# Optimization experiments

Hardware: AMD Instinct MI355X
Metric: run time of the kernel (lower is better)

Reference implementation:

```python
import math
import jax, jax.numpy as jnp
import numpy as np

B, N, D, Pd, L, H = 2, 384, 256, 64, 8, 8
Dh = D // H
VOCAB = 21


def _layernorm(x, w, b, eps=1e-5):
    m = jnp.mean(x, axis=-1, keepdims=True)
    v = jnp.var(x, axis=-1, keepdims=True)
    return (x - m) * jax.lax.rsqrt(v + eps) * w + b


def _safe_norm(v):
    return jnp.sqrt(jnp.sum(v * v, axis=-1, keepdims=True) + 1e-8)


def _rot6d(r6):
    # Zhou et al. 6D rotation -> 3x3 via Gram-Schmidt (rows b1,b2,b3)
    a1, a2 = r6[..., :3], r6[..., 3:6]
    b1 = a1 / _safe_norm(a1)
    a2p = a2 - jnp.sum(b1 * a2, axis=-1, keepdims=True) * b1
    b2 = a2p / _safe_norm(a2p)
    b3 = jnp.cross(b1, b2)
    return jnp.stack([b1, b2, b3], axis=-2)  # [..., 3, 3]


def _pos_enc(n, d):
    pos = jnp.arange(n, dtype=jnp.float32)[:, None]
    div = jnp.exp(jnp.arange(0, d, 2, dtype=jnp.float32) * (-math.log(10000.0) / d))
    ang = pos * div  # [n, d/2]
    return jnp.zeros((n, d), jnp.float32).at[:, 0::2].set(jnp.sin(ang)).at[:, 1::2].set(jnp.cos(ang))


def _se3_frame_attention(Q, K, V, frames):
    # Frame-conditioned attention: dot-product scores biased by squared
    # distance between frame translations (IPA-style point bias).
    t = frames[..., :3, 3]                                   # [B,N,3]
    d2 = jnp.sum((t[:, :, None] - t[:, None, :]) ** 2, -1)   # [B,N,N]
    s = jnp.einsum('bihd,bjhd->bhij', Q, K) / math.sqrt(Dh) - d2[:, None]
    a = jax.nn.softmax(s, axis=-1)
    return jnp.einsum('bhij,bjhd->bihd', a, V)               # [B,N,H,Dh]


def _encode(tokens, tok_emb, emb_ln_w, emb_ln_b, Wq, Wk, Wv, Wo, bo,
            attn_ln_w, attn_ln_b, ff_ln_w, ff_ln_b, W1, b1, W2, b2,
            Wop, bop, relpos_emb, pair_ln_w, pair_ln_b, Wf1, bf1, Wf2, bf2):
    Bb, Nn = tokens.shape
    x = tok_emb[tokens] + _pos_enc(Nn, D)[None]
    x = _layernorm(x, emb_ln_w, emb_ln_b)
    frames = jnp.broadcast_to(jnp.eye(4, dtype=x.dtype), (Bb, Nn, 4, 4))
    pos = jnp.arange(Nn)
    rel = jnp.clip(pos[None, :] - pos[:, None], -64, 64) + 64  # rel[i,j]=pos[j]-pos[i]
    rel_e = relpos_emb[rel]                                    # [N,N,Pd]
    bot = jnp.broadcast_to(jnp.array([0.0, 0.0, 0.0, 1.0], x.dtype), (Bb, Nn, 1, 4))
    for l in range(L):
        # SE3 attention block (dropout = identity in eval)
        Q = (x @ Wq[l]).reshape(Bb, Nn, H, Dh)
        Kh = (x @ Wk[l]).reshape(Bb, Nn, H, Dh)
        Vh = (x @ Wv[l]).reshape(Bb, Nn, H, Dh)
        ao = _se3_frame_attention(Q, Kh, Vh, frames).reshape(Bb, Nn, D)
        x = _layernorm(x + ao @ Wo[l] + bo[l], attn_ln_w[l], attn_ln_b[l])
        # FFN (pre-LN inside the Sequential), residual add
        h = _layernorm(x, ff_ln_w[l], ff_ln_b[l])
        x = x + (jax.nn.gelu(h @ W1[l] + b1[l], approximate=False) @ W2[l] + b2[l])
        # Pair features
        proj = jax.nn.relu(x @ Wop + bop)                      # [B,N,Pd]
        pair = _layernorm(proj[:, :, None] + proj[:, None, :] + rel_e[None],
                          pair_ln_w, pair_ln_b)                # [B,N,N,Pd]
        # Frame head
        feat = jnp.concatenate([x, pair.mean(axis=2)], axis=-1)
        raw = jax.nn.silu(feat @ Wf1 + bf1) @ Wf2 + bf2        # [B,N,9]
        R = _rot6d(raw[..., :6])
        trans = raw[..., 6:]
        top = jnp.concatenate([R, trans[..., None]], axis=-1)  # [B,N,3,4]
        frames = jnp.concatenate([top, bot], axis=-2)          # [B,N,4,4]
    return frames, x


def setup_inputs() -> dict:
    key = jax.random.key(0)
    ks = iter(jax.random.split(key, 16))
    def w(shape, scale):
        return (jax.random.normal(next(ks), shape) * scale).astype(jnp.float32)
    return {
        'tokens': jax.random.randint(next(ks), (B, N), 0, VOCAB, dtype=jnp.int32),
        'tok_emb': w((VOCAB, D), 0.02),
        'emb_ln_w': jnp.ones((D,), jnp.float32), 'emb_ln_b': jnp.zeros((D,), jnp.float32),
        'Wq': w((L, D, D), D ** -0.5), 'Wk': w((L, D, D), D ** -0.5),
        'Wv': w((L, D, D), D ** -0.5), 'Wo': w((L, D, D), D ** -0.5),
        'bo': jnp.zeros((L, D), jnp.float32),
        'attn_ln_w': jnp.ones((L, D), jnp.float32), 'attn_ln_b': jnp.zeros((L, D), jnp.float32),
        'ff_ln_w': jnp.ones((L, D), jnp.float32), 'ff_ln_b': jnp.zeros((L, D), jnp.float32),
        'W1': w((L, D, 4 * D), D ** -0.5), 'b1': jnp.zeros((L, 4 * D), jnp.float32),
        'W2': w((L, 4 * D, D), (4 * D) ** -0.5), 'b2': jnp.zeros((L, D), jnp.float32),
        'Wop': w((D, Pd), D ** -0.5), 'bop': jnp.zeros((Pd,), jnp.float32),
        'relpos_emb': w((129, Pd), 0.02),
        'pair_ln_w': jnp.ones((Pd,), jnp.float32), 'pair_ln_b': jnp.zeros((Pd,), jnp.float32),
        'Wf1': w((D + Pd, 128), (D + Pd) ** -0.5), 'bf1': jnp.zeros((128,), jnp.float32),
        'Wf2': w((128, 9), 128 ** -0.5), 'bf2': jnp.zeros((9,), jnp.float32),
    }


def reference(tokens, tok_emb, emb_ln_w, emb_ln_b, Wq, Wk, Wv, Wo, bo,
              attn_ln_w, attn_ln_b, ff_ln_w, ff_ln_b, W1, b1, W2, b2,
              Wop, bop, relpos_emb, pair_ln_w, pair_ln_b, Wf1, bf1, Wf2, bf2):
    return _encode(tokens, tok_emb, emb_ln_w, emb_ln_b, Wq, Wk, Wv, Wo, bo,
                   attn_ln_w, attn_ln_b, ff_ln_w, ff_ln_b, W1, b1, W2, b2,
                   Wop, bop, relpos_emb, pair_ln_w, pair_ln_b, Wf1, bf1, Wf2, bf2)
```

## Files before the change

kernel.cpp:

```cpp
#include <hip/hip_runtime.h>
#include <hip/hip_bf16.h>
#include <math.h>

#define B_  2
#define N_  384
#define D_  256
#define PD_ 64
#define L_  8
#define H_  8
#define DH_ 32
#define GR  4
#define IT  8
#define RT_ 132

__global__ void prologue_kernel(const int* __restrict__ tokens, const float* __restrict__ tok_emb,
                                const float* __restrict__ lnw, const float* __restrict__ lnb,
                                const float* __restrict__ relpos,
                                float* __restrict__ x, float* __restrict__ frames,
                                float* __restrict__ tx, float* __restrict__ ty,
                                float* __restrict__ tz,
                                float* __restrict__ relc, float* __restrict__ relcT) {
  int row = blockIdx.x;
  int n = row % N_;
  int d = threadIdx.x;
  __shared__ float rbuf[256];
  __shared__ float smr;
  if (d < 16) frames[row * 16 + d] = (d == 0 || d == 5 || d == 10 || d == 15) ? 1.0f : 0.0f;
  if (d == 16) tx[row] = 0.0f;
  if (d == 17) ty[row] = 0.0f;
  if (d == 18) tz[row] = 0.0f;
  if (row < 129 && d >= 192) {
    int lane = d & 63;
    float s = relpos[row * PD_ + lane];
    #pragma unroll
    for (int off = 32; off >= 1; off >>= 1) s += __shfl_xor(s, off, 64);
    if (lane == 0) smr = s * (1.0f / PD_);
  }
  int tok = tokens[row];
  float val = tok_emb[tok * D_ + d];
  int i = d >> 1;
  float dv = expf((float)(2 * i) * (-logf(10000.0f) / (float)D_));
  float ang = (float)n * dv;
  val += (d & 1) ? cosf(ang) : sinf(ang);
  rbuf[d] = val; __syncthreads();
  for (int s = 128; s > 0; s >>= 1) { if (d < s) rbuf[d] += rbuf[d + s]; __syncthreads(); }
  float mean = rbuf[0] / D_;
  __syncthreads();
  rbuf[d] = val * val; __syncthreads();
  for (int s = 128; s > 0; s >>= 1) { if (d < s) rbuf[d] += rbuf[d + s]; __syncthreads(); }
  float var = rbuf[0] / D_ - mean * mean;
  float r = rsqrtf(var + 1e-5f);
  x[row * D_ + d] = (val - mean) * r * lnw[d] + lnb[d];
  if (row < 129 && d < PD_) {
    float cv = relpos[row * PD_ + d] - smr;
    relc[row * PD_ + d] = cv;
    relcT[d * RT_ + row] = cv;
  }
}

__device__ __forceinline__ void qkv_unit(int bid, int tid, const float* __restrict__ x,
                                         const float* __restrict__ Wq, const float* __restrict__ Wk,
                                         const float* __restrict__ Wv,
                                         float* __restrict__ q, float* __restrict__ kt,
                                         float* __restrict__ v, float* sA) {
  int tile = bid & 3;
  int m = (bid >> 2) % 3;
  int r0 = (bid / 12) * GR;
  float* red = sA + GR * D_;
  {
    int r = tid >> 6, lane = tid & 63;
    ((float4*)(sA + r * D_))[lane] = ((const float4*)(x + (size_t)(r0 + r) * D_))[lane];
  }
  __syncthreads();
  const float* W = (m == 0) ? Wq : (m == 1) ? Wk : Wv;
  int kc = tid >> 6, c = tid & 63;
  const float* wp = W + (size_t)(kc * 64) * D_ + tile * 64 + c;
  const float* s0 = sA + kc * 64;
  float a0 = 0.f, a1 = 0.f, a2 = 0.f, a3 = 0.f;
  for (int kk = 0; kk < 64; kk += 4) {
    float w0 = wp[(size_t)kk * D_], w1 = wp[(size_t)(kk + 1) * D_];
    float w2 = wp[(size_t)(kk + 2) * D_], w3 = wp[(size_t)(kk + 3) * D_];
    float4 h0 = *(const float4*)(s0 + 0 * D_ + kk);
    float4 h1 = *(const float4*)(s0 + 1 * D_ + kk);
    float4 h2 = *(const float4*)(s0 + 2 * D_ + kk);
    float4 h3 = *(const float4*)(s0 + 3 * D_ + kk);
    a0 = fmaf(h0.x, w0, fmaf(h0.y, w1, fmaf(h0.z, w2, fmaf(h0.w, w3, a0))));
    a1 = fmaf(h1.x, w0, fmaf(h1.y, w1, fmaf(h1.z, w2, fmaf(h1.w, w3, a1))));
    a2 = fmaf(h2.x, w0, fmaf(h2.y, w1, fmaf(h2.z, w2, fmaf(h2.w, w3, a2))));
    a3 = fmaf(h3.x, w0, fmaf(h3.y, w1, fmaf(h3.z, w2, fmaf(h3.w, w3, a3))));
  }
  red[(kc * 4 + 0) * 64 + c] = a0;
  red[(kc * 4 + 1) * 64 + c] = a1;
  red[(kc * 4 + 2) * 64 + c] = a2;
  red[(kc * 4 + 3) * 64 + c] = a3;
  __syncthreads();
  int r = tid >> 6;
  float s = red[(0 * 4 + r) * 64 + c] + red[(1 * 4 + r) * 64 + c]
          + red[(2 * 4 + r) * 64 + c] + red[(3 * 4 + r) * 64 + c];
  int col = tile * 64 + c;
  int row = r0 + r;
  if (m == 1) {
    int b = row / N_, j = row % N_;
    int hh = col >> 5, dd = col & 31;
    kt[((size_t)(b * H_ + hh) * DH_ + dd) * N_ + j] = s;
  } else {
    float* O = (m == 0) ? q : v;
    O[(size_t)row * D_ + col] = s;
  }
}

__device__ __forceinline__ void proj_unit(int row, int tid, const float* __restrict__ x,
                                          const float* __restrict__ Wop, const float* __restrict__ bop,
                                          float* __restrict__ projc, float* __restrict__ projcT,
                                          float* smem) {
  float* sA  = smem;
  float* red = smem + 256;
  if (tid < 64) ((float4*)sA)[tid] = ((const float4*)(x + (size_t)row * D_))[tid];
  __syncthreads();
  int kc = tid >> 6, c = tid & 63;
  const float* wp = Wop + (kc * 64) * PD_ + c;
  const float* s0 = sA + kc * 64;
  float a0 = 0.f, a1 = 0.f, a2 = 0.f, a3 = 0.f;
  for (int kk = 0; kk < 64; kk += 4) {
    a0 = fmaf(s0[kk],     wp[(kk)     * PD_], a0);
    a1 = fmaf(s0[kk + 1], wp[(kk + 1) * PD_], a1);
    a2 = fmaf(s0[kk + 2], wp[(kk + 2) * PD_], a2);
    a3 = fmaf(s0[kk + 3], wp[(kk + 3) * PD_], a3);
  }
  red[kc * 64 + c] = (a0 + a1) + (a2 + a3);
  __syncthreads();
  if (tid < 64) {
    float acc = fmaxf(bop[tid] + red[tid] + red[64 + tid] + red[128 + tid] + red[192 + tid], 0.0f);
    float s = acc;
    #pragma unroll
    for (int off = 32; off >= 1; off >>= 1) s += __shfl_xor(s, off, 64);
    float cv = acc - s * (1.0f / PD_);
    projc[row * PD_ + tid] = cv;
    projcT[(size_t)tid * (B_ * N_) + row] = cv;
  }
}

__global__ void qkv_kernel(const float* __restrict__ x, const float* __restrict__ Wq,
                           const float* __restrict__ Wk, const float* __restrict__ Wv,
                           float* __restrict__ q, float* __restrict__ kt, float* __restrict__ v) {
  __shared__ __align__(16) float smem[2048];
  qkv_unit(blockIdx.x, threadIdx.x, x, Wq, Wk, Wv, q, kt, v, smem);
}

__global__ void proj_qkv_kernel(const float* __restrict__ x,
                                const float* __restrict__ Wop, const float* __restrict__ bop,
                                float* __restrict__ projc, float* __restrict__ projcT,
                                const float* __restrict__ Wq, const float* __restrict__ Wk,
                                const float* __restrict__ Wv,
                                float* __restrict__ q, float* __restrict__ kt,
                                float* __restrict__ v) {
  __shared__ __align__(16) float smem[2048];
  int bid = blockIdx.x, tid = threadIdx.x;
  if (bid < B_ * N_) proj_unit(bid, tid, x, Wop, bop, projc, projcT, smem);
  else               qkv_unit(bid - B_ * N_, tid, x, Wq, Wk, Wv, q, kt, v, smem);
}

__global__ void wo_ln_kernel(const float* __restrict__ ao, const float* __restrict__ Wo,
                             const float* __restrict__ bo,
                             const float* __restrict__ lnw, const float* __restrict__ lnb,
                             float* __restrict__ x) {
  int r0 = blockIdx.x * 2;
  int tid = threadIdx.x;
  int wave = tid >> 6, lane = tid & 63;
  __shared__ __align__(16) float sAO[2 * D_];
  __shared__ float wred[4][4];
  if (tid < 128) ((float4*)sAO)[tid] = ((const float4*)(ao + (size_t)r0 * D_))[tid];
  __syncthreads();
  const float* wp = Wo + tid;
  float a0 = 0.f, a1 = 0.f, a2 = 0.f, a3 = 0.f;
  float c0 = 0.f, c1 = 0.f, c2 = 0.f, c3 = 0.f;
  for (int kk = 0; kk < D_; kk += 4) {
    float w0 = wp[(size_t)kk * D_], w1 = wp[(size_t)(kk + 1) * D_];
    float w2 = wp[(size_t)(kk + 2) * D_], w3 = wp[(size_t)(kk + 3) * D_];
    float4 h0 = *(const float4*)(sAO + kk);
    float4 h1 = *(const float4*)(sAO + D_ + kk);
    a0 = fmaf(h0.x, w0, a0); a1 = fmaf(h0.y, w1, a1);
    a2 = fmaf(h0.z, w2, a2); a3 = fmaf(h0.w, w3, a3);
    c0 = fmaf(h1.x, w0, c0); c1 = fmaf(h1.y, w1, c1);
    c2 = fmaf(h1.z, w2, c2); c3 = fmaf(h1.w, w3, c3);
  }
  float bb = bo[tid];
  float v0 = x[(size_t)r0 * D_ + tid]       + bb + (a0 + a1) + (a2 + a3);
  float v1 = x[(size_t)(r0 + 1) * D_ + tid] + bb + (c0 + c1) + (c2 + c3);
  float s0 = v0, q0 = v0 * v0, s1 = v1, q1 = v1 * v1;
  #pragma unroll
  for (int off = 32; off >= 1; off >>= 1) {
    s0 += __shfl_xor(s0, off, 64); q0 += __shfl_xor(q0, off, 64);
    s1 += __shfl_xor(s1, off, 64); q1 += __shfl_xor(q1, off, 64);
  }
  if (lane == 0) {
    wred[0][wave] = s0; wred[1][wave] = q0;
    wred[2][wave] = s1; wred[3][wave] = q1;
  }
  __syncthreads();
  float S0 = wred[0][0] + wred[0][1] + wred[0][2] + wred[0][3];
  float Q0 = wred[1][0] + wred[1][1] + wred[1][2] + wred[1][3];
  float S1 = wred[2][0] + wred[2][1] + wred[2][2] + wred[2][3];
  float Q1 = wred[3][0] + wred[3][1] + wred[3][2] + wred[3][3];
  float m0 = S0 * (1.0f / D_), m1 = S1 * (1.0f / D_);
  float r0v = rsqrtf(Q0 * (1.0f / D_) - m0 * m0 + 1e-5f);
  float r1v = rsqrtf(Q1 * (1.0f / D_) - m1 * m1 + 1e-5f);
  float wv = lnw[tid], bv = lnb[tid];
  x[(size_t)r0 * D_ + tid]       = (v0 - m0) * r0v * wv + bv;
  x[(size_t)(r0 + 1) * D_ + tid] = (v1 - m1) * r1v * wv + bv;
}

__global__ void gemm4t_kernel(const float* __restrict__ A, const float* __restrict__ W,
                              const float* __restrict__ bias, const float* __restrict__ resid,
                              float* __restrict__ C, int K, int Nc) {
  int tiles = Nc >> 5;
  int bid = blockIdx.x;
  int tile = bid % tiles;
  int r0 = (bid / tiles) * GR;
  int tid = threadIdx.x;
  extern __shared__ __align__(16) float sA[];
  float* red = sA + GR * K;
  {
    int r = tid >> 6, lane = tid & 63;
    for (int kk = lane; kk < (K >> 2); kk += 64)
      ((float4*)(sA + r * K))[kk] = ((const float4*)(A + (size_t)(r0 + r) * K))[kk];
  }
  __syncthreads();
  int kc = tid >> 5, c = tid & 31;
  int KC = K >> 3;
  const float* wp = W + (size_t)(kc * KC) * Nc + tile * 32 + c;
  const float* s0 = sA + kc * KC;
  float a0 = 0.f, a1 = 0.f, a2 = 0.f, a3 = 0.f;
  for (int kk = 0; kk < KC; kk += 4) {
    float w0 = wp[(size_t)kk * Nc], w1 = wp[(size_t)(kk + 1) * Nc];
    float w2 = wp[(size_t)(kk + 2) * Nc], w3 = wp[(size_t)(kk + 3) * Nc];
    float4 h0 = *(const float4*)(s0 + 0 * K + kk);
    float4 h1 = *(const float4*)(s0 + 1 * K + kk);
    float4 h2 = *(const float4*)(s0 + 2 * K + kk);
    float4 h3 = *(const float4*)(s0 + 3 * K + kk);
    a0 = fmaf(h0.x, w0, fmaf(h0.y, w1, fmaf(h0.z, w2, fmaf(h0.w, w3, a0))));
    a1 = fmaf(h1.x, w0, fmaf(h1.y, w1, fmaf(h1.z, w2, fmaf(h1.w, w3, a1))));
    a2 = fmaf(h2.x, w0, fmaf(h2.y, w1, fmaf(h2.z, w2, fmaf(h2.w, w3, a2))));
    a3 = fmaf(h3.x, w0, fmaf(h3.y, w1, fmaf(h3.z, w2, fmaf(h3.w, w3, a3))));
  }
  red[(kc * 4 + 0) * 32 + c] = a0;
  red[(kc * 4 + 1) * 32 + c] = a1;
  red[(kc * 4 + 2) * 32 + c] = a2;
  red[(kc * 4 + 3) * 32 + c] = a3;
  __syncthreads();
  if (tid < GR * 32) {
    int r = tid >> 5, cc = tid & 31;
    float s = 0.f;
    #pragma unroll
    for (int k8 = 0; k8 < 8; k8++) s += red[(k8 * 4 + r) * 32 + cc];
    int col = tile * 32 + cc;
    if (bias)  s += bias[col];
    if (resid) s += resid[(size_t)(r0 + r) * Nc + col];
    C[(size_t)(r0 + r) * Nc + col] = s;
  }
}

__global__ void ff1_kernel(const float* __restrict__ x,
                           const float* __restrict__ lnw, const float* __restrict__ lnb,
                           const float* __restrict__ W1, const float* __restrict__ b1,
                           float* __restrict__ f) {
  int bid = blockIdx.x;
  int tile = bid & 7;
  int r0 = (bid >> 3) * GR;
  int tid = threadIdx.x;
  __shared__ __align__(16) float sA[GR * D_];
  __shared__ float red[2 * GR * 128];
  {
    int r = tid >> 6, lane = tid & 63;
    float4 v = ((const float4*)(x + (size_t)(r0 + r) * D_))[lane];
    float s = v.x + v.y + v.z + v.w;
    float s2 = v.x * v.x + v.y * v.y + v.z * v.z + v.w * v.w;
    #pragma unroll
    for (int off = 32; off >= 1; off >>= 1) {
      s  += __shfl_xor(s, off, 64);
      s2 += __shfl_xor(s2, off, 64);
    }
    float mean = s * (1.0f / D_);
    float var = s2 * (1.0f / D_) - mean * mean;
    float rin = rsqrtf(var + 1e-5f);
    float4 w4 = ((const float4*)lnw)[lane];
    float4 b4 = ((const float4*)lnb)[lane];
    float4 nv;
    nv.x = (v.x - mean) * rin * w4.x + b4.x;
    nv.y = (v.y - mean) * rin * w4.y + b4.y;
    nv.z = (v.z - mean) * rin * w4.z + b4.z;
    nv.w = (v.w - mean) * rin * w4.w + b4.w;
    ((float4*)(sA + r * D_))[lane] = nv;
  }
  __syncthreads();
  int kc = tid >> 7, c = tid & 127;
  int col = tile * 128 + c;
  const float* wp = W1 + (size_t)(kc * 128) * 1024 + col;
  const float* s0 = sA + kc * 128;
  float a0 = 0.f, a1 = 0.f, a2 = 0.f, a3 = 0.f;
  for (int kk = 0; kk < 128; kk += 4) {
    float w0 = wp[(size_t)kk * 1024], w1 = wp[(size_t)(kk + 1) * 1024];
    float w2 = wp[(size_t)(kk + 2) * 1024], w3 = wp[(size_t)(kk + 3) * 1024];
    float4 h0 = *(const float4*)(s0 + 0 * D_ + kk);
    float4 h1 = *(const float4*)(s0 + 1 * D_ + kk);
    float4 h2 = *(const float4*)(s0 + 2 * D_ + kk);
    float4 h3 = *(const float4*)(s0 + 3 * D_ + kk);
    a0 = fmaf(h0.x, w0, fmaf(h0.y, w1, fmaf(h0.z, w2, fmaf(h0.w, w3, a0))));
    a1 = fmaf(h1.x, w0, fmaf(h1.y, w1, fmaf(h1.z, w2, fmaf(h1.w, w3, a1))));
    a2 = fmaf(h2.x, w0, fmaf(h2.y, w1, fmaf(h2.z, w2, fmaf(h2.w, w3, a2))));
    a3 = fmaf(h3.x, w0, fmaf(h3.y, w1, fmaf(h3.z, w2, fmaf(h3.w, w3, a3))));
  }
  red[(kc * 4 + 0) * 128 + c] = a0;
  red[(kc * 4 + 1) * 128 + c] = a1;
  red[(kc * 4 + 2) * 128 + c] = a2;
  red[(kc * 4 + 3) * 128 + c] = a3;
  __syncthreads();
  int rA = tid >> 7;
  #pragma unroll
  for (int p = 0; p < 2; p++) {
    int r = rA + p * 2;
    float s = red[(0 * 4 + r) * 128 + c] + red[(1 * 4 + r) * 128 + c] + b1[col];
    s = 0.5f * s * (1.0f + erff(s * 0.7071067811865475f));
    f[(size_t)(r0 + r) * 1024 + col] = s;
  }
}

__global__ void attn_kernel(const float* __restrict__ Q, const float* __restrict__ KT,
                            const float* __restrict__ V,
                            const float* __restrict__ tx, const float* __restrict__ ty,
                            const float* __restrict__ tz, float* __restrict__ AO) {
  const int TILES = N_ / IT;
  int bid = blockIdx.x;
  int it = bid % TILES;
  int h  = (bid / TILES) % H_;
  int b  = bid / (TILES * H_);
  int i0 = it * IT;
  int tid = threadIdx.x;
  int wave = tid >> 6, lane = tid & 63;

  __shared__ __align__(16) float sQ[IT * DH_];
  __shared__ __align__(16) float sK[DH_ * 64];
  __shared__ __align__(16) float sV[64 * DH_];
  __shared__ float sS[IT][N_];
  __shared__ float sti[3][IT];
  __shared__ float sinv[IT];

  {
    int ii = tid >> 5, d = tid & 31;
    sQ[ii * DH_ + d] = Q[((size_t)(b * N_ + i0 + ii)) * D_ + h * DH_ + d];
  }
  if (tid < IT) {
    sti[0][tid] = tx[b * N_ + i0 + tid];
    sti[1][tid] = ty[b * N_ + i0 + tid];
    sti[2][tid] = tz[b * N_ + i0 + tid];
  }
  const float* ktb = KT + (size_t)(b * H_ + h) * DH_ * N_;
  const float* vb  = V + (size_t)b * N_ * D_ + h * DH_;
  const float* txb = tx + b * N_;
  const float* tyb = ty + b * N_;
  const float* tzb = tz + b * N_;
  __syncthreads();

  for (int jc = 0; jc < N_; jc += 64) {
    for (int idx = tid; idx < DH_ * 64; idx += 256) {
      int d = idx >> 6, jj = idx & 63;
      sK[d * 64 + jj] = ktb[(size_t)d * N_ + jc + jj];
    }
    __syncthreads();
    int jj = lane;
    float tjx = txb[jc + jj], tjy = tyb[jc + jj], tjz = tzb[jc + jj];
    const float* q0 = sQ + (wave * 2 + 0) * DH_;
    const float* q1 = sQ + (wave * 2 + 1) * DH_;
    float a0 = 0.f, a1 = 0.f;
    #pragma unroll 8
    for (int d = 0; d < DH_; d++) {
      float kv = sK[d * 64 + jj];
      a0 = fmaf(q0[d], kv, a0);
      a1 = fmaf(q1[d], kv, a1);
    }
    #pragma unroll
    for (int s = 0; s < 2; s++) {
      int ii = wave * 2 + s;
      float a = (s == 0) ? a0 : a1;
      float dx = sti[0][ii] - tjx;
      float dy = sti[1][ii] - tjy;
      float dz = sti[2][ii] - tjz;
      sS[ii][jc + jj] = a * 0.17677669529663689f - (dx * dx + dy * dy + dz * dz);
    }
    __syncthreads();
  }

  #pragma unroll
  for (int s = 0; s < 2; s++) {
    int ii = wave * 2 + s;
    float vrow[6];
    float m = -1e30f;
    #pragma unroll
    for (int t = 0; t < 6; t++) { vrow[t] = sS[ii][t * 64 + lane]; m = fmaxf(m, vrow[t]); }
    #pragma unroll
    for (int off = 32; off >= 1; off >>= 1) m = fmaxf(m, __shfl_xor(m, off, 64));
    float ps = 0.f;
    #pragma unroll
    for (int t = 0; t < 6; t++) {
      float e = expf(vrow[t] - m);
      sS[ii][t * 64 + lane] = e;
      ps += e;
    }
    #pragma unroll
    for (int off = 32; off >= 1; off >>= 1) ps += __shfl_xor(ps, off, 64);
    if (lane == 0) sinv[ii] = 1.0f / ps;
  }
  __syncthreads();

  int ii = tid >> 5, dd = tid & 31;
  float o0 = 0.f, o1 = 0.f;
  for (int jc = 0; jc < N_; jc += 64) {
    for (int idx = tid; idx < 64 * DH_; idx += 256) {
      int jj = idx >> 5, d = idx & 31;
      sV[jj * DH_ + d] = vb[(size_t)(jc + jj) * D_ + d];
    }
    __syncthreads();
    #pragma unroll 8
    for (int jj = 0; jj < 64; jj += 2) {
      o0 = fmaf(sS[ii][jc + jj],     sV[jj * DH_ + dd],       o0);
      o1 = fmaf(sS[ii][jc + jj + 1], sV[(jj + 1) * DH_ + dd], o1);
    }
    __syncthreads();
  }
  AO[((size_t)(b * N_ + i0 + ii)) * D_ + h * DH_ + dd] = (o0 + o1) * sinv[ii];
}

__global__ void pair_head_kernel(const float* __restrict__ projc, const float* __restrict__ projcT,
                                 const float* __restrict__ relc, const float* __restrict__ relcT,
                                 const float* __restrict__ lnw, const float* __restrict__ lnb,
                                 const float* __restrict__ x,
                                 const float* __restrict__ Wf1, const float* __restrict__ bWf1,
                                 const float* __restrict__ Wf2, const float* __restrict__ bWf2,
                                 float* __restrict__ frames, float* __restrict__ tx,
                                 float* __restrict__ ty, float* __restrict__ tz) {
  const int M = B_ * N_;
  int row = blockIdx.x;
  int b = row / N_;
  int i = row % N_;
  int tid = threadIdx.x;
  int lane = tid & 63;
  int wave = tid >> 6;
  __shared__ float svpi[PD_];
  __shared__ float sr[N_];
  __shared__ float red[4][PD_];
  __shared__ float sfeat[320];
  __shared__ float fred[2][128];
  __shared__ float sg[128];
  __shared__ float sraw[9];

  if (tid < PD_) svpi[tid] = projc[row * PD_ + tid];
  if (tid < D_) sfeat[tid] = x[(size_t)row * D_ + tid];
  __syncthreads();

  {
    int jA = tid;
    int raA = jA - i; raA = raA < -64 ? -64 : (raA > 64 ? 64 : raA); raA += 64;
    const float* pA = projcT + b * N_ + jA;
    const float* rA = relcT + raA;
    float s2A = 0.f;
    #pragma unroll 8
    for (int c = 0; c < PD_; c++) {
      float dA = svpi[c] + pA[(size_t)c * M] + rA[c * RT_];
      s2A = fmaf(dA, dA, s2A);
    }
    sr[jA] = rsqrtf(s2A * (1.0f / PD_) + 1e-5f);
    if (tid < 128) {
      int jB = tid + 256;
      int raB = jB - i; raB = raB < -64 ? -64 : (raB > 64 ? 64 : raB); raB += 64;
      const float* pB = projcT + b * N_ + jB;
      const float* rB = relcT + raB;
      float s2B = 0.f;
      #pragma unroll 8
      for (int c = 0; c < PD_; c++) {
        float dB = svpi[c] + pB[(size_t)c * M] + rB[c * RT_];
        s2B = fmaf(dB, dB, s2B);
      }
      sr[jB] = rsqrtf(s2B * (1.0f / PD_) + 1e-5f);
    }
  }
  __syncthreads();

  {
    float vpl = svpi[lane];
    const float* pb = projc + (size_t)b * N_ * PD_;
    float acc = 0.0f;
    for (int j = wave * 2; j < N_; j += 8) {
      int ja = j, jb = j + 1;
      int ra = ja - i; ra = ra < -64 ? -64 : (ra > 64 ? 64 : ra); ra += 64;
      int rb = jb - i; rb = rb < -64 ? -64 : (rb > 64 ? 64 : rb); rb += 64;
      float da = vpl + pb[ja * PD_ + lane] + relc[ra * PD_ + lane];
      float db = vpl + pb[jb * PD_ + lane] + relc[rb * PD_ + lane];
      acc = fmaf(da, sr[ja], fmaf(db, sr[jb], acc));
    }
    red[wave][lane] = acc;
  }
  __syncthreads();
  if (wave == 0) {
    float s = red[0][lane] + red[1][lane] + red[2][lane] + red[3][lane];
    sfeat[D_ + lane] = lnb[lane] + s * lnw[lane] * (1.0f / N_);
  }
  __syncthreads();

  int kc = tid >> 7, c = tid & 127;
  int koff = kc * 160;
  const float* wp = Wf1 + (size_t)koff * 128 + c;
  const float* s0 = sfeat + koff;
  float a0 = 0.f, a1 = 0.f, a2 = 0.f, a3 = 0.f;
  for (int kk = 0; kk < 160; kk += 4) {
    a0 = fmaf(s0[kk],     wp[(size_t)kk * 128],       a0);
    a1 = fmaf(s0[kk + 1], wp[(size_t)(kk + 1) * 128], a1);
    a2 = fmaf(s0[kk + 2], wp[(size_t)(kk + 2) * 128], a2);
    a3 = fmaf(s0[kk + 3], wp[(size_t)(kk + 3) * 128], a3);
  }
  fred[kc][c] = (a0 + a1) + (a2 + a3);
  __syncthreads();
  if (tid < 128) {
    float g = fred[0][tid] + fred[1][tid] + bWf1[tid];
    sg[tid] = g / (1.0f + expf(-g));
  }
  __syncthreads();

  if (tid < 9) {
    float b0 = 0.f, b1v = 0.f;
    for (int kk = 0; kk < 128; kk += 2) {
      b0  = fmaf(sg[kk],     Wf2[(kk)     * 9 + tid], b0);
      b1v = fmaf(sg[kk + 1], Wf2[(kk + 1) * 9 + tid], b1v);
    }
    sraw[tid] = bWf2[tid] + b0 + b1v;
  }
  __syncthreads();
  if (tid == 0) {
    float a1x = sraw[0], a1y = sraw[1], a1z = sraw[2];
    float a2x = sraw[3], a2y = sraw[4], a2z = sraw[5];
    float n1 = sqrtf(a1x * a1x + a1y * a1y + a1z * a1z + 1e-8f);
    float b1x = a1x / n1, b1y = a1y / n1, b1z = a1z / n1;
    float dp = b1x * a2x + b1y * a2y + b1z * a2z;
    float px = a2x - dp * b1x, py = a2y - dp * b1y, pz = a2z - dp * b1z;
    float n2 = sqrtf(px * px + py * py + pz * pz + 1e-8f);
    float b2x = px / n2, b2y = py / n2, b2z = pz / n2;
    float b3x = b1y * b2z - b1z * b2y;
    float b3y = b1z * b2x - b1x * b2z;
    float b3z = b1x * b2y - b1y * b2x;
    float* f = frames + row * 16;
    f[0]  = b1x; f[1]  = b1y; f[2]  = b1z; f[3]  = sraw[6];
    f[4]  = b2x; f[5]  = b2y; f[6]  = b2z; f[7]  = sraw[7];
    f[8]  = b3x; f[9]  = b3y; f[10] = b3z; f[11] = sraw[8];
    f[12] = 0.0f; f[13] = 0.0f; f[14] = 0.0f; f[15] = 1.0f;
    tx[row] = sraw[6];
    ty[row] = sraw[7];
    tz[row] = sraw[8];
  }
}

__global__ void write_out_kernel(const float* __restrict__ frames, const float* __restrict__ x,
                                 float* __restrict__ out) {
  int i = blockIdx.x * 256 + threadIdx.x;
  const int nf = B_ * N_ * 16;
  const int total = nf + B_ * N_ * D_;
  if (i < nf) out[i] = frames[i];
  else if (i < total) out[i] = x[i - nf];
}

extern "C" void kernel_launch(void* const* d_in, const int* in_sizes, int n_in,
                              void* d_out, int out_size, void* d_ws, size_t ws_size,
                              hipStream_t stream) {
  const int*   tokens    = (const int*)  d_in[0];
  const float* tok_emb   = (const float*)d_in[1];
  const float* emb_ln_w  = (const float*)d_in[2];
  const float* emb_ln_b  = (const float*)d_in[3];
  const float* Wq        = (const float*)d_in[4];
  const float* Wk        = (const float*)d_in[5];
  const float* Wv        = (const float*)d_in[6];
  const float* Wo        = (const float*)d_in[7];
  const float* bo        = (const float*)d_in[8];
  const float* attn_ln_w = (const float*)d_in[9];
  const float* attn_ln_b = (const float*)d_in[10];
  const float* ff_ln_w   = (const float*)d_in[11];
  const float* ff_ln_b   = (const float*)d_in[12];
  const float* W1        = (const float*)d_in[13];
  const float* b1        = (const float*)d_in[14];
  const float* W2        = (const float*)d_in[15];
  const float* b2        = (const float*)d_in[16];
  const float* Wop       = (const float*)d_in[17];
  const float* bop       = (const float*)d_in[18];
  const float* relpos    = (const float*)d_in[19];
  const float* pair_ln_w = (const float*)d_in[20];
  const float* pair_ln_b = (const float*)d_in[21];
  const float* Wf1       = (const float*)d_in[22];
  const float* bWf1      = (const float*)d_in[23];
  const float* Wf2       = (const float*)d_in[24];
  const float* bWf2      = (const float*)d_in[25];

  const int M = B_ * N_;
  const int XE = M * D_;
  float* ws     = (float*)d_ws;
  float* frames = ws;
  float* projc  = frames + M * 16;
  float* projcT = projc  + M * PD_;
  float* relc   = projcT + M * PD_;
  float* relcT  = relc   + 8320;
  float* tx     = relcT  + 8448;
  float* ty     = tx     + M;
  float* tz     = ty     + M;
  float* x      = tz     + M;
  float* q      = x  + XE;
  float* kt     = q  + XE;
  float* v      = kt + XE;
  float* ao     = v  + XE;
  float* f      = q;

  prologue_kernel<<<M, 256, 0, stream>>>(tokens, tok_emb, emb_ln_w, emb_ln_b, relpos,
                                         x, frames, tx, ty, tz, relc, relcT);
  qkv_kernel<<<(M / GR) * 12, 256, 0, stream>>>(x, Wq, Wk, Wv, q, kt, v);

  const size_t lds_ff2 = (GR * 1024 + 1024) * sizeof(float);

  for (int l = 0; l < L_; l++) {
    attn_kernel<<<B_ * H_ * (N_ / IT), 256, 0, stream>>>(q, kt, v, tx, ty, tz, ao);
    wo_ln_kernel<<<M / 2, 256, 0, stream>>>(ao, Wo + (size_t)l * D_ * D_, bo + l * D_,
                                            attn_ln_w + l * D_, attn_ln_b + l * D_, x);
    ff1_kernel<<<(M / GR) * 8, 256, 0, stream>>>(x, ff_ln_w + l * D_, ff_ln_b + l * D_,
                                                 W1 + (size_t)l * D_ * 1024, b1 + l * 1024, f);
    gemm4t_kernel<<<(M / GR) * 8, 256, lds_ff2, stream>>>(
        f, W2 + (size_t)l * 1024 * D_, b2 + l * D_, x, x, 1024, D_);
    if (l < L_ - 1) {
      int lq = l + 1;
      proj_qkv_kernel<<<M + (M / GR) * 12, 256, 0, stream>>>(
          x, Wop, bop, projc, projcT,
          Wq + (size_t)lq * D_ * D_, Wk + (size_t)lq * D_ * D_, Wv + (size_t)lq * D_ * D_,
          q, kt, v);
    } else {
      proj_qkv_kernel<<<M, 256, 0, stream>>>(x, Wop, bop, projc, projcT, Wq, Wk, Wv, q, kt, v);
    }
    pair_head_kernel<<<M, 256, 0, stream>>>(projc, projcT, relc, relcT, pair_ln_w, pair_ln_b,
                                            x, Wf1, bWf1, Wf2, bWf2, frames, tx, ty, tz);
  }

  const int total = B_ * N_ * 16 + B_ * N_ * D_;
  write_out_kernel<<<(total + 255) / 256, 256, 0, stream>>>(frames, x, (float*)d_out);
}
```

Measured before the change: 1.016 ms.

## Widen GEMM column tiles per thread and register-cache Q in attention

The QKV, FF1 and FF2 GEMM kernels now compute twice as many output columns per thread, which halves their grid sizes and reuses each LDS-loaded activation across two weight columns. The Wo kernel switches to a split-K layout with an LDS reduction. The attention kernel keeps Q rows in registers as float4 and reads score rows as float4 in the PV loop. The intent is to cut shared-memory traffic and loop overhead per FMA, at the cost of fewer blocks (lower parallelism on a small M=768 problem), more registers and more LDS per block.

```diff
diff --git a/kernel.cpp b/kernel.cpp
--- a/kernel.cpp
+++ b/kernel.cpp
@@ -63,9 +63,9 @@
                                          const float* __restrict__ Wv,
                                          float* __restrict__ q, float* __restrict__ kt,
                                          float* __restrict__ v, float* sA) {
-  int tile = bid & 3;
-  int m = (bid >> 2) % 3;
-  int r0 = (bid / 12) * GR;
+  int tile = bid & 1;
+  int m = (bid >> 1) % 3;
+  int r0 = (bid / 6) * GR;
   float* red = sA + GR * D_;
   {
     int r = tid >> 6, lane = tid & 63;
@@ -74,38 +74,53 @@
   __syncthreads();
   const float* W = (m == 0) ? Wq : (m == 1) ? Wk : Wv;
   int kc = tid >> 6, c = tid & 63;
-  const float* wp = W + (size_t)(kc * 64) * D_ + tile * 64 + c;
+  const float* wp = W + (size_t)(kc * 64) * D_ + tile * 128 + c;
   const float* s0 = sA + kc * 64;
   float a0 = 0.f, a1 = 0.f, a2 = 0.f, a3 = 0.f;
+  float b0 = 0.f, b1 = 0.f, b2 = 0.f, b3 = 0.f;
   for (int kk = 0; kk < 64; kk += 4) {
-    float w0 = wp[(size_t)kk * D_], w1 = wp[(size_t)(kk + 1) * D_];
-    float w2 = wp[(size_t)(kk + 2) * D_], w3 = wp[(size_t)(kk + 3) * D_];
+    float u0 = wp[(size_t)kk * D_],       u1 = wp[(size_t)(kk + 1) * D_];
+    float u2 = wp[(size_t)(kk + 2) * D_], u3 = wp[(size_t)(kk + 3) * D_];
+    float w0 = wp[(size_t)kk * D_ + 64],       w1 = wp[(size_t)(kk + 1) * D_ + 64];
+    float w2 = wp[(size_t)(kk + 2) * D_ + 64], w3 = wp[(size_t)(kk + 3) * D_ + 64];
     float4 h0 = *(const float4*)(s0 + 0 * D_ + kk);
     float4 h1 = *(const float4*)(s0 + 1 * D_ + kk);
     float4 h2 = *(const float4*)(s0 + 2 * D_ + kk);
     float4 h3 = *(const float4*)(s0 + 3 * D_ + kk);
-    a0 = fmaf(h0.x, w0, fmaf(h0.y, w1, fmaf(h0.z, w2, fmaf(h0.w, w3, a0))));
-    a1 = fmaf(h1.x, w0, fmaf(h1.y, w1, fmaf(h1.z, w2, fmaf(h1.w, w3, a1))));
-    a2 = fmaf(h2.x, w0, fmaf(h2.y, w1, fmaf(h2.z, w2, fmaf(h2.w, w3, a2))));
-    a3 = fmaf(h3.x, w0, fmaf(h3.y, w1, fmaf(h3.z, w2, fmaf(h3.w, w3, a3))));
-  }
-  red[(kc * 4 + 0) * 64 + c] = a0;
-  red[(kc * 4 + 1) * 64 + c] = a1;
-  red[(kc * 4 + 2) * 64 + c] = a2;
-  red[(kc * 4 + 3) * 64 + c] = a3;
+    a0 = fmaf(h0.x, u0, fmaf(h0.y, u1, fmaf(h0.z, u2, fmaf(h0.w, u3, a0))));
+    a1 = fmaf(h1.x, u0, fmaf(h1.y, u1, fmaf(h1.z, u2, fmaf(h1.w, u3, a1))));
+    a2 = fmaf(h2.x, u0, fmaf(h2.y, u1, fmaf(h2.z, u2, fmaf(h2.w, u3, a2))));
+    a3 = fmaf(h3.x, u0, fmaf(h3.y, u1, fmaf(h3.z, u2, fmaf(h3.w, u3, a3))));
+    b0 = fmaf(h0.x, w0, fmaf(h0.y, w1, fmaf(h0.z, w2, fmaf(h0.w, w3, b0))));
+    b1 = fmaf(h1.x, w0, fmaf(h1.y, w1, fmaf(h1.z, w2, fmaf(h1.w, w3, b1))));
+    b2 = fmaf(h2.x, w0, fmaf(h2.y, w1, fmaf(h2.z, w2, fmaf(h2.w, w3, b2))));
+    b3 = fmaf(h3.x, w0, fmaf(h3.y, w1, fmaf(h3.z, w2, fmaf(h3.w, w3, b3))));
+  }
+  red[(kc * 4 + 0) * 128 + c] = a0;
+  red[(kc * 4 + 1) * 128 + c] = a1;
+  red[(kc * 4 + 2) * 128 + c] = a2;
+  red[(kc * 4 + 3) * 128 + c] = a3;
+  red[(kc * 4 + 0) * 128 + 64 + c] = b0;
+  red[(kc * 4 + 1) * 128 + 64 + c] = b1;
+  red[(kc * 4 + 2) * 128 + 64 + c] = b2;
+  red[(kc * 4 + 3) * 128 + 64 + c] = b3;
   __syncthreads();
   int r = tid >> 6;
-  float s = red[(0 * 4 + r) * 64 + c] + red[(1 * 4 + r) * 64 + c]
-          + red[(2 * 4 + r) * 64 + c] + red[(3 * 4 + r) * 64 + c];
-  int col = tile * 64 + c;
+  float s = red[(0 * 4 + r) * 128 + c] + red[(1 * 4 + r) * 128 + c]
+          + red[(2 * 4 + r) * 128 + c] + red[(3 * 4 + r) * 128 + c];
+  float s2 = red[(0 * 4 + r) * 128 + 64 + c] + red[(1 * 4 + r) * 128 + 64 + c]
+           + red[(2 * 4 + r) * 128 + 64 + c] + red[(3 * 4 + r) * 128 + 64 + c];
   int row = r0 + r;
+  int col0 = tile * 128 + c;
+  int col1 = col0 + 64;
   if (m == 1) {
     int b = row / N_, j = row % N_;
-    int hh = col >> 5, dd = col & 31;
-    kt[((size_t)(b * H_ + hh) * DH_ + dd) * N_ + j] = s;
+    kt[((size_t)(b * H_ + (col0 >> 5)) * DH_ + (col0 & 31)) * N_ + j] = s;
+    kt[((size_t)(b * H_ + (col1 >> 5)) * DH_ + (col1 & 31)) * N_ + j] = s2;
   } else {
     float* O = (m == 0) ? q : v;
-    O[(size_t)row * D_ + col] = s;
+    O[(size_t)row * D_ + col0] = s;
+    O[(size_t)row * D_ + col1] = s2;
   }
 }
 
@@ -143,7 +158,7 @@
 __global__ void qkv_kernel(const float* __restrict__ x, const float* __restrict__ Wq,
                            const float* __restrict__ Wk, const float* __restrict__ Wv,
                            float* __restrict__ q, float* __restrict__ kt, float* __restrict__ v) {
-  __shared__ __align__(16) float smem[2048];
+  __shared__ __align__(16) float smem[3072];
   qkv_unit(blockIdx.x, threadIdx.x, x, Wq, Wk, Wv, q, kt, v, smem);
 }
 
@@ -154,7 +169,7 @@
                                 const float* __restrict__ Wv,
                                 float* __restrict__ q, float* __restrict__ kt,
                                 float* __restrict__ v) {
-  __shared__ __align__(16) float smem[2048];
+  __shared__ __align__(16) float smem[3072];
   int bid = blockIdx.x, tid = threadIdx.x;
   if (bid < B_ * N_) proj_unit(bid, tid, x, Wop, bop, projc, projcT, smem);
   else               qkv_unit(bid - B_ * N_, tid, x, Wq, Wk, Wv, q, kt, v, smem);
@@ -168,25 +183,37 @@
   int tid = threadIdx.x;
   int wave = tid >> 6, lane = tid & 63;
   __shared__ __align__(16) float sAO[2 * D_];
+  __shared__ float red[4 * D_];
   __shared__ float wred[4][4];
   if (tid < 128) ((float4*)sAO)[tid] = ((const float4*)(ao + (size_t)r0 * D_))[tid];
   __syncthreads();
-  const float* wp = Wo + tid;
-  float a0 = 0.f, a1 = 0.f, a2 = 0.f, a3 = 0.f;
-  float c0 = 0.f, c1 = 0.f, c2 = 0.f, c3 = 0.f;
-  for (int kk = 0; kk < D_; kk += 4) {
-    float w0 = wp[(size_t)kk * D_], w1 = wp[(size_t)(kk + 1) * D_];
-    float w2 = wp[(size_t)(kk + 2) * D_], w3 = wp[(size_t)(kk + 3) * D_];
-    float4 h0 = *(const float4*)(sAO + kk);
-    float4 h1 = *(const float4*)(sAO + D_ + kk);
-    a0 = fmaf(h0.x, w0, a0); a1 = fmaf(h0.y, w1, a1);
-    a2 = fmaf(h0.z, w2, a2); a3 = fmaf(h0.w, w3, a3);
-    c0 = fmaf(h1.x, w0, c0); c1 = fmaf(h1.y, w1, c1);
-    c2 = fmaf(h1.z, w2, c2); c3 = fmaf(h1.w, w3, c3);
-  }
+  {
+    int kc = tid >> 7, c = tid & 127;
+    const float* wp = Wo + (size_t)(kc * 128) * D_ + c;
+    const float* s0 = sAO + kc * 128;
+    const float* s1 = sAO + D_ + kc * 128;
+    float a0 = 0.f, a1 = 0.f, b0v = 0.f, b1v = 0.f;
+    for (int kk = 0; kk < 128; kk += 4) {
+      float u0 = wp[(size_t)kk * D_],       u1 = wp[(size_t)(kk + 1) * D_];
+      float u2 = wp[(size_t)(kk + 2) * D_], u3 = wp[(size_t)(kk + 3) * D_];
+      float w0 = wp[(size_t)kk * D_ + 128],       w1 = wp[(size_t)(kk + 1) * D_ + 128];
+      float w2 = wp[(size_t)(kk + 2) * D_ + 128], w3 = wp[(size_t)(kk + 3) * D_ + 128];
+      float4 h0 = *(const float4*)(s0 + kk);
+      float4 h1 = *(const float4*)(s1 + kk);
+      a0  = fmaf(h0.x, u0, fmaf(h0.y, u1, fmaf(h0.z, u2, fmaf(h0.w, u3, a0))));
+      a1  = fmaf(h1.x, u0, fmaf(h1.y, u1, fmaf(h1.z, u2, fmaf(h1.w, u3, a1))));
+      b0v = fmaf(h0.x, w0, fmaf(h0.y, w1, fmaf(h0.z, w2, fmaf(h0.w, w3, b0v))));
+      b1v = fmaf(h1.x, w0, fmaf(h1.y, w1, fmaf(h1.z, w2, fmaf(h1.w, w3, b1v))));
+    }
+    red[(kc * 2 + 0) * D_ + c] = a0;
+    red[(kc * 2 + 1) * D_ + c] = a1;
+    red[(kc * 2 + 0) * D_ + 128 + c] = b0v;
+    red[(kc * 2 + 1) * D_ + 128 + c] = b1v;
+  }
+  __syncthreads();
   float bb = bo[tid];
-  float v0 = x[(size_t)r0 * D_ + tid]       + bb + (a0 + a1) + (a2 + a3);
-  float v1 = x[(size_t)(r0 + 1) * D_ + tid] + bb + (c0 + c1) + (c2 + c3);
+  float v0 = x[(size_t)r0 * D_ + tid]       + bb + red[0 * D_ + tid] + red[2 * D_ + tid];
+  float v1 = x[(size_t)(r0 + 1) * D_ + tid] + bb + red[1 * D_ + tid] + red[3 * D_ + tid];
   float s0 = v0, q0 = v0 * v0, s1 = v1, q1 = v1 * v1;
   #pragma unroll
   for (int off = 32; off >= 1; off >>= 1) {
@@ -213,7 +240,7 @@
 __global__ void gemm4t_kernel(const float* __restrict__ A, const float* __restrict__ W,
                               const float* __restrict__ bias, const float* __restrict__ resid,
                               float* __restrict__ C, int K, int Nc) {
-  int tiles = Nc >> 5;
+  int tiles = Nc >> 6;
   int bid = blockIdx.x;
   int tile = bid % tiles;
   int r0 = (bid / tiles) * GR;
@@ -228,32 +255,43 @@
   __syncthreads();
   int kc = tid >> 5, c = tid & 31;
   int KC = K >> 3;
-  const float* wp = W + (size_t)(kc * KC) * Nc + tile * 32 + c;
+  const float* wp = W + (size_t)(kc * KC) * Nc + tile * 64 + c;
   const float* s0 = sA + kc * KC;
   float a0 = 0.f, a1 = 0.f, a2 = 0.f, a3 = 0.f;
+  float b0 = 0.f, b1 = 0.f, b2 = 0.f, b3 = 0.f;
   for (int kk = 0; kk < KC; kk += 4) {
-    float w0 = wp[(size_t)kk * Nc], w1 = wp[(size_t)(kk + 1) * Nc];
-    float w2 = wp[(size_t)(kk + 2) * Nc], w3 = wp[(size_t)(kk + 3) * Nc];
+    float u0 = wp[(size_t)kk * Nc],       u1 = wp[(size_t)(kk + 1) * Nc];
+    float u2 = wp[(size_t)(kk + 2) * Nc], u3 = wp[(size_t)(kk + 3) * Nc];
+    float w0 = wp[(size_t)kk * Nc + 32],       w1 = wp[(size_t)(kk + 1) * Nc + 32];
+    float w2 = wp[(size_t)(kk + 2) * Nc + 32], w3 = wp[(size_t)(kk + 3) * Nc + 32];
     float4 h0 = *(const float4*)(s0 + 0 * K + kk);
     float4 h1 = *(const float4*)(s0 + 1 * K + kk);
     float4 h2 = *(const float4*)(s0 + 2 * K + kk);
     float4 h3 = *(const float4*)(s0 + 3 * K + kk);
-    a0 = fmaf(h0.x, w0, fmaf(h0.y, w1, fmaf(h0.z, w2, fmaf(h0.w, w3, a0))));
-    a1 = fmaf(h1.x, w0, fmaf(h1.y, w1, fmaf(h1.z, w2, fmaf(h1.w, w3, a1))));
-    a2 = fmaf(h2.x, w0, fmaf(h2.y, w1, fmaf(h2.z, w2, fmaf(h2.w, w3, a2))));
-    a3 = fmaf(h3.x, w0, fmaf(h3.y, w1, fmaf(h3.z, w2, fmaf(h3.w, w3, a3))));
-  }
-  red[(kc * 4 + 0) * 32 + c] = a0;
-  red[(kc * 4 + 1) * 32 + c] = a1;
-  red[(kc * 4 + 2) * 32 + c] = a2;
-  red[(kc * 4 + 3) * 32 + c] = a3;
-  __syncthreads();
-  if (tid < GR * 32) {
-    int r = tid >> 5, cc = tid & 31;
+    a0 = fmaf(h0.x, u0, fmaf(h0.y, u1, fmaf(h0.z, u2, fmaf(h0.w, u3, a0))));
+    a1 = fmaf(h1.x, u0, fmaf(h1.y, u1, fmaf(h1.z, u2, fmaf(h1.w, u3, a1))));
+    a2 = fmaf(h2.x, u0, fmaf(h2.y, u1, fmaf(h2.z, u2, fmaf(h2.w, u3, a2))));
+    a3 = fmaf(h3.x, u0, fmaf(h3.y, u1, fmaf(h3.z, u2, fmaf(h3.w, u3, a3))));
+    b0 = fmaf(h0.x, w0, fmaf(h0.y, w1, fmaf(h0.z, w2, fmaf(h0.w, w3, b0))));
+    b1 = fmaf(h1.x, w0, fmaf(h1.y, w1, fmaf(h1.z, w2, fmaf(h1.w, w3, b1))));
+    b2 = fmaf(h2.x, w0, fmaf(h2.y, w1, fmaf(h2.z, w2, fmaf(h2.w, w3, b2))));
+    b3 = fmaf(h3.x, w0, fmaf(h3.y, w1, fmaf(h3.z, w2, fmaf(h3.w, w3, b3))));
+  }
+  red[(kc * 4 + 0) * 64 + c] = a0;
+  red[(kc * 4 + 1) * 64 + c] = a1;
+  red[(kc * 4 + 2) * 64 + c] = a2;
+  red[(kc * 4 + 3) * 64 + c] = a3;
+  red[(kc * 4 + 0) * 64 + 32 + c] = b0;
+  red[(kc * 4 + 1) * 64 + 32 + c] = b1;
+  red[(kc * 4 + 2) * 64 + 32 + c] = b2;
+  red[(kc * 4 + 3) * 64 + 32 + c] = b3;
+  __syncthreads();
+  {
+    int r = tid >> 6, cc = tid & 63;
     float s = 0.f;
     #pragma unroll
-    for (int k8 = 0; k8 < 8; k8++) s += red[(k8 * 4 + r) * 32 + cc];
-    int col = tile * 32 + cc;
+    for (int k8 = 0; k8 < 8; k8++) s += red[(k8 * 4 + r) * 64 + cc];
+    int col = tile * 64 + cc;
     if (bias)  s += bias[col];
     if (resid) s += resid[(size_t)(r0 + r) * Nc + col];
     C[(size_t)(r0 + r) * Nc + col] = s;
@@ -265,11 +303,11 @@
                            const float* __restrict__ W1, const float* __restrict__ b1,
                            float* __restrict__ f) {
   int bid = blockIdx.x;
-  int tile = bid & 7;
-  int r0 = (bid >> 3) * GR;
+  int tile = bid & 3;
+  int r0 = (bid >> 2) * GR;
   int tid = threadIdx.x;
   __shared__ __align__(16) float sA[GR * D_];
-  __shared__ float red[2 * GR * 128];
+  __shared__ float red[2 * GR * 256];
   {
     int r = tid >> 6, lane = tid & 63;
     float4 v = ((const float4*)(x + (size_t)(r0 + r) * D_))[lane];
@@ -294,32 +332,44 @@
   }
   __syncthreads();
   int kc = tid >> 7, c = tid & 127;
-  int col = tile * 128 + c;
-  const float* wp = W1 + (size_t)(kc * 128) * 1024 + col;
+  int col0 = tile * 256 + c;
+  const float* wp = W1 + (size_t)(kc * 128) * 1024 + col0;
   const float* s0 = sA + kc * 128;
   float a0 = 0.f, a1 = 0.f, a2 = 0.f, a3 = 0.f;
+  float b0 = 0.f, b1v = 0.f, b2 = 0.f, b3 = 0.f;
   for (int kk = 0; kk < 128; kk += 4) {
-    float w0 = wp[(size_t)kk * 1024], w1 = wp[(size_t)(kk + 1) * 1024];
-    float w2 = wp[(size_t)(kk + 2) * 1024], w3 = wp[(size_t)(kk + 3) * 1024];
+    float u0 = wp[(size_t)kk * 1024],       u1 = wp[(size_t)(kk + 1) * 1024];
+    float u2 = wp[(size_t)(kk + 2) * 1024], u3 = wp[(size_t)(kk + 3) * 1024];
+    float w0 = wp[(size_t)kk * 1024 + 128],       w1 = wp[(size_t)(kk + 1) * 1024 + 128];
+    float w2 = wp[(size_t)(kk + 2) * 1024 + 128], w3 = wp[(size_t)(kk + 3) * 1024 + 128];
     float4 h0 = *(const float4*)(s0 + 0 * D_ + kk);
     float4 h1 = *(const float4*)(s0 + 1 * D_ + kk);
     float4 h2 = *(const float4*)(s0 + 2 * D_ + kk);
     float4 h3 = *(const float4*)(s0 + 3 * D_ + kk);
-    a0 = fmaf(h0.x, w0, fmaf(h0.y, w1, fmaf(h0.z, w2, fmaf(h0.w, w3, a0))));
-    a1 = fmaf(h1.x, w0, fmaf(h1.y, w1, fmaf(h1.z, w2, fmaf(h1.w, w3, a1))));
-    a2 = fmaf(h2.x, w0, fmaf(h2.y, w1, fmaf(h2.z, w2, fmaf(h2.w, w3, a2))));
-    a3 = fmaf(h3.x, w0, fmaf(h3.y, w1, fmaf(h3.z, w2, fmaf(h3.w, w3, a3))));
-  }
-  red[(kc * 4 + 0) * 128 + c] = a0;
-  red[(kc * 4 + 1) * 128 + c] = a1;
-  red[(kc * 4 + 2) * 128 + c] = a2;
-  red[(kc * 4 + 3) * 128 + c] = a3;
-  __syncthreads();
-  int rA = tid >> 7;
+    a0  = fmaf(h0.x, u0, fmaf(h0.y, u1, fmaf(h0.z, u2, fmaf(h0.w, u3, a0))));
+    a1  = fmaf(h1.x, u0, fmaf(h1.y, u1, fmaf(h1.z, u2, fmaf(h1.w, u3, a1))));
+    a2  = fmaf(h2.x, u0, fmaf(h2.y, u1, fmaf(h2.z, u2, fmaf(h2.w, u3, a2))));
+    a3  = fmaf(h3.x, u0, fmaf(h3.y, u1, fmaf(h3.z, u2, fmaf(h3.w, u3, a3))));
+    b0  = fmaf(h0.x, w0, fmaf(h0.y, w1, fmaf(h0.z, w2, fmaf(h0.w, w3, b0))));
+    b1v = fmaf(h1.x, w0, fmaf(h1.y, w1, fmaf(h1.z, w2, fmaf(h1.w, w3, b1v))));
+    b2  = fmaf(h2.x, w0, fmaf(h2.y, w1, fmaf(h2.z, w2, fmaf(h2.w, w3, b2))));
+    b3  = fmaf(h3.x, w0, fmaf(h3.y, w1, fmaf(h3.z, w2, fmaf(h3.w, w3, b3))));
+  }
+  red[(kc * 4 + 0) * 256 + c] = a0;
+  red[(kc * 4 + 1) * 256 + c] = a1;
+  red[(kc * 4 + 2) * 256 + c] = a2;
+  red[(kc * 4 + 3) * 256 + c] = a3;
+  red[(kc * 4 + 0) * 256 + 128 + c] = b0;
+  red[(kc * 4 + 1) * 256 + 128 + c] = b1v;
+  red[(kc * 4 + 2) * 256 + 128 + c] = b2;
+  red[(kc * 4 + 3) * 256 + 128 + c] = b3;
+  __syncthreads();
+  int r = tid >> 6, cc = tid & 63;
   #pragma unroll
-  for (int p = 0; p < 2; p++) {
-    int r = rA + p * 2;
-    float s = red[(0 * 4 + r) * 128 + c] + red[(1 * 4 + r) * 128 + c] + b1[col];
+  for (int p = 0; p < 4; p++) {
+    int off = p * 64 + cc;
+    int col = tile * 256 + off;
+    float s = red[(0 * 4 + r) * 256 + off] + red[(1 * 4 + r) * 256 + off] + b1[col];
     s = 0.5f * s * (1.0f + erff(s * 0.7071067811865475f));
     f[(size_t)(r0 + r) * 1024 + col] = s;
   }
@@ -341,7 +391,7 @@
   __shared__ __align__(16) float sQ[IT * DH_];
   __shared__ __align__(16) float sK[DH_ * 64];
   __shared__ __align__(16) float sV[64 * DH_];
-  __shared__ float sS[IT][N_];
+  __shared__ __align__(16) float sS[IT][N_];
   __shared__ float sti[3][IT];
   __shared__ float sinv[IT];
 
@@ -361,6 +411,13 @@
   const float* tzb = tz + b * N_;
   __syncthreads();
 
+  float4 q0r[8], q1r[8];
+  #pragma unroll
+  for (int t = 0; t < 8; t++) {
+    q0r[t] = ((const float4*)(sQ + (wave * 2 + 0) * DH_))[t];
+    q1r[t] = ((const float4*)(sQ + (wave * 2 + 1) * DH_))[t];
+  }
+
   for (int jc = 0; jc < N_; jc += 64) {
     for (int idx = tid; idx < DH_ * 64; idx += 256) {
       int d = idx >> 6, jj = idx & 63;
@@ -369,14 +426,16 @@
     __syncthreads();
     int jj = lane;
     float tjx = txb[jc + jj], tjy = tyb[jc + jj], tjz = tzb[jc + jj];
-    const float* q0 = sQ + (wave * 2 + 0) * DH_;
-    const float* q1 = sQ + (wave * 2 + 1) * DH_;
     float a0 = 0.f, a1 = 0.f;
-    #pragma unroll 8
-    for (int d = 0; d < DH_; d++) {
-      float kv = sK[d * 64 + jj];
-      a0 = fmaf(q0[d], kv, a0);
-      a1 = fmaf(q1[d], kv, a1);
+    #pragma unroll
+    for (int t = 0; t < 8; t++) {
+      float k0 = sK[(4 * t + 0) * 64 + jj];
+      float k1 = sK[(4 * t + 1) * 64 + jj];
+      float k2 = sK[(4 * t + 2) * 64 + jj];
+      float k3 = sK[(4 * t + 3) * 64 + jj];
+      float4 qa = q0r[t], qb = q1r[t];
+      a0 = fmaf(qa.x, k0, fmaf(qa.y, k1, fmaf(qa.z, k2, fmaf(qa.w, k3, a0))));
+      a1 = fmaf(qb.x, k0, fmaf(qb.y, k1, fmaf(qb.z, k2, fmaf(qb.w, k3, a1))));
     }
     #pragma unroll
     for (int s = 0; s < 2; s++) {
@@ -420,10 +479,14 @@
       sV[jj * DH_ + d] = vb[(size_t)(jc + jj) * D_ + d];
     }
     __syncthreads();
-    #pragma unroll 8
-    for (int jj = 0; jj < 64; jj += 2) {
-      o0 = fmaf(sS[ii][jc + jj],     sV[jj * DH_ + dd],       o0);
-      o1 = fmaf(sS[ii][jc + jj + 1], sV[(jj + 1) * DH_ + dd], o1);
+    const float* srow = &sS[ii][jc];
+    #pragma unroll
+    for (int jj = 0; jj < 64; jj += 4) {
+      float4 sv = *(const float4*)(srow + jj);
+      o0 = fmaf(sv.x, sV[(jj + 0) * DH_ + dd], o0);
+      o1 = fmaf(sv.y, sV[(jj + 1) * DH_ + dd], o1);
+      o0 = fmaf(sv.z, sV[(jj + 2) * DH_ + dd], o0);
+      o1 = fmaf(sv.w, sV[(jj + 3) * DH_ + dd], o1);
     }
     __syncthreads();
   }
@@ -616,21 +679,21 @@
 
   prologue_kernel<<<M, 256, 0, stream>>>(tokens, tok_emb, emb_ln_w, emb_ln_b, relpos,
                                          x, frames, tx, ty, tz, relc, relcT);
-  qkv_kernel<<<(M / GR) * 12, 256, 0, stream>>>(x, Wq, Wk, Wv, q, kt, v);
-
-  const size_t lds_ff2 = (GR * 1024 + 1024) * sizeof(float);
+  qkv_kernel<<<(M / GR) * 6, 256, 0, stream>>>(x, Wq, Wk, Wv, q, kt, v);
+
+  const size_t lds_ff2 = (GR * 1024 + 2048) * sizeof(float);
 
   for (int l = 0; l < L_; l++) {
     attn_kernel<<<B_ * H_ * (N_ / IT), 256, 0, stream>>>(q, kt, v, tx, ty, tz, ao);
     wo_ln_kernel<<<M / 2, 256, 0, stream>>>(ao, Wo + (size_t)l * D_ * D_, bo + l * D_,
                                             attn_ln_w + l * D_, attn_ln_b + l * D_, x);
-    ff1_kernel<<<(M / GR) * 8, 256, 0, stream>>>(x, ff_ln_w + l * D_, ff_ln_b + l * D_,
+    ff1_kernel<<<(M / GR) * 4, 256, 0, stream>>>(x, ff_ln_w + l * D_, ff_ln_b + l * D_,
                                                  W1 + (size_t)l * D_ * 1024, b1 + l * 1024, f);
-    gemm4t_kernel<<<(M / GR) * 8, 256, lds_ff2, stream>>>(
+    gemm4t_kernel<<<(M / GR) * 4, 256, lds_ff2, stream>>>(
         f, W2 + (size_t)l * 1024 * D_, b2 + l * D_, x, x, 1024, D_);
     if (l < L_ - 1) {
       int lq = l + 1;
-      proj_qkv_kernel<<<M + (M / GR) * 12, 256, 0, stream>>>(
+      proj_qkv_kernel<<<M + (M / GR) * 6, 256, 0, stream>>>(
           x, Wop, bop, projc, projcT,
           Wq + (size_t)lq * D_ * D_, Wk + (size_t)lq * D_ * D_, Wv + (size_t)lq * D_ * D_,
           q, kt, v);
```

Measured after the change: 1.103 ms. 8.5% more time.
